# Optimization experiments

Measured on AMD Instinct MI355X. Metric: run time of the kernel, lower is better.

The kernel has to match this reference:

```python
import jax, jax.numpy as jnp
import numpy as np

BETA = 1.0

def setup_inputs() -> dict:
    key = jax.random.key(0)
    k1, k2 = jax.random.split(key)
    z = jax.random.normal(k1, (8, 8192, 64), dtype=jnp.float32)
    # codebook initialized as randn * sc (sc=0.001) in the original module
    codebook = jax.random.normal(k2, (1024, 64), dtype=jnp.float32) * 0.001
    return {"z": z, "codebook": codebook}

def reference(z, codebook):
    # squared euclidean distances: ||z||^2 + ||c||^2 - 2 z.c  -> [B, T, code_num]
    d = (jnp.sum(z ** 2, axis=-1, keepdims=True)
         + jnp.sum(codebook ** 2, axis=1)
         - 2.0 * jnp.einsum('btd,kd->btk', z, codebook))
    min_encoding_indices = jnp.argmin(d, axis=-1)            # [B, T] int
    # one-hot @ codebook is exactly a gather of nearest code vectors
    z_q = codebook[min_encoding_indices]                     # [B, T, D]
    sg = jax.lax.stop_gradient
    loss = jnp.mean((sg(z_q) - z) ** 2) + BETA * jnp.mean((z_q - sg(z)) ** 2)
    # straight-through estimator
    z_q_st = z + sg(z_q - z)
    return (z_q_st, min_encoding_indices, loss)
```

## Files before the change

kernel.cpp:

```cpp
#include <hip/hip_runtime.h>

#define TOKENS 65536
#define DIM 64
#define NCODE 1024
#define MARGIN 1e-5f
#define MARGINS (MARGIN * 2097152.0f)
#define FLAG_CAP 4096
#define TPG 8

#define OUT_IDX_OFF ((size_t)TOKENS * DIM)
#define OUT_LOSS_OFF (OUT_IDX_OFF + TOKENS)

#define WS_LOSS   0
#define WS_FLAGC  8
#define WS_DONEA  12
#define WS_DGRP   16
#define WS_BNORM  2064
#define WS_BNS    6160
#define WS_CHI    10256
#define WS_CLO    141328
#define WS_PACKED 272400
#define WS_FLAGS  337936

typedef __attribute__((ext_vector_type(8))) short short8;
typedef __attribute__((ext_vector_type(8))) _Float16 half8;
typedef __attribute__((ext_vector_type(4))) float f32x4;

static __device__ __forceinline__ half8 as_h8(short8 v) {
    return __builtin_bit_cast(half8, v);
}

__device__ __forceinline__ float np_sumsq64(const float* __restrict__ x) {
#pragma clang fp contract(off)
    float r[8];
#pragma unroll
    for (int j = 0; j < 8; ++j) r[j] = x[j] * x[j];
#pragma unroll
    for (int i = 8; i < 64; i += 8) {
#pragma unroll
        for (int j = 0; j < 8; ++j) {
            float sq = x[i + j] * x[i + j];
            r[j] = r[j] + sq;
        }
    }
    return ((r[0] + r[1]) + (r[2] + r[3])) + ((r[4] + r[5]) + (r[6] + r[7]));
}

__global__ __launch_bounds__(256) void vq_prep(
    const float* __restrict__ cb, unsigned short* __restrict__ chi,
    unsigned short* __restrict__ clo, float* __restrict__ bnorm,
    float* __restrict__ bns,
    unsigned int* __restrict__ ctrl ) {
    int tid = blockIdx.x * 256 + threadIdx.x;
    if (tid < 516) ctrl[tid] = 0u;
    int j = tid & 7;
    int L = (tid >> 3) & 63;
    int cs = tid >> 9;
    int s = cs & 1, c = cs >> 1;
    int code = c * 16 + (L & 15);
    int d = s * 32 + (L >> 4) * 8 + j;
    float v = -8192.0f * cb[(size_t)code * DIM + d];
    _Float16 h = (_Float16)v;
    float hf = (float)h;
    float lo;
    {
#pragma clang fp contract(off)
        lo = v - hf;
    }
    _Float16 l = (_Float16)lo;
    chi[tid] = __builtin_bit_cast(unsigned short, h);
    clo[tid] = __builtin_bit_cast(unsigned short, l);

    if (tid < NCODE) {
        float bn = np_sumsq64(cb + (size_t)tid * DIM);
        bnorm[tid] = bn;
        bns[tid] = bn * 2097152.0f;
    }
}

__device__ __forceinline__ void top2_merge(float& a1, float& a2, int& ai,
                                           float b1, float b2, int bi) {
    float n1 = fminf(a1, b1);
    float n2 = fminf(fmaxf(a1, b1), fminf(a2, b2));
    ai = (b1 < a1) ? bi : ai;
    a1 = n1; a2 = n2;
}

__global__ __launch_bounds__(256, 4) void vq_fast(
    const float* __restrict__ z, const float* __restrict__ cb,
    const unsigned short* __restrict__ cfrag_hi,
    const unsigned short* __restrict__ cfrag_lo,
    const float* __restrict__ bnorm_s, float* __restrict__ out,
    unsigned int* __restrict__ flag_count, int* __restrict__ flag_list,
    unsigned long long* __restrict__ packed_min,
    double* __restrict__ loss_sum, unsigned int flag_cap) {
    __shared__ short8 sh_hi[2][512];
    __shared__ short8 sh_lo[2][512];
    __shared__ float bn_lds[NCODE];
    __shared__ int s_best[64];
    __shared__ int s_flag[64];

    const int tid = threadIdx.x;
    const int lane = tid & 63;
    const int w = tid >> 6;
    const int t0 = blockIdx.x * 64;
    const int tw = t0 + w * 16;
    const int col = lane & 15;
    const int quad = lane >> 4;

    ((float4*)bn_lds)[tid] = ((const float4*)bnorm_s)[tid];

    half8 zhi[2], zlo[2];
#pragma unroll
    for (int s = 0; s < 2; ++s) {
        const float* zp = z + (size_t)(tw + col) * DIM + s * 32 + quad * 8;
        float4 f0 = ((const float4*)zp)[0];
        float4 f1 = ((const float4*)zp)[1];
        float f[8] = {f0.x, f0.y, f0.z, f0.w, f1.x, f1.y, f1.z, f1.w};
        half8 hh8, ll8;
#pragma unroll
        for (int j = 0; j < 8; ++j) {
            float sv = f[j] * 512.0f;
            _Float16 hh = (_Float16)sv;
            float hf = (float)hh;
            float lo;
            {
#pragma clang fp contract(off)
                lo = sv - hf;
            }
            hh8[j] = hh;
            ll8[j] = (_Float16)lo;
        }
        zhi[s] = hh8; zlo[s] = ll8;
    }

    const short8* CH = (const short8*)cfrag_hi;
    const short8* CL = (const short8*)cfrag_lo;

    {
        short8 a0 = CH[tid], a1 = CH[tid + 256];
        short8 b0 = CL[tid], b1 = CL[tid + 256];
        sh_hi[0][tid] = a0; sh_hi[0][tid + 256] = a1;
        sh_lo[0][tid] = b0; sh_lo[0][tid + 256] = b1;
    }
    __syncthreads();

    float m1 = 3.0e38f, m2 = 3.0e38f;
    int bi = 0;
    const int koff = quad * 4;

    for (int g = 0; g < 16; ++g) {
        const int buf = g & 1;
        short8 a0, a1, b0, b1;
        if (g < 15) {
            const int base = (g + 1) * 512 + tid;
            a0 = CH[base]; a1 = CH[base + 256];
            b0 = CL[base]; b1 = CL[base + 256];
        }
#pragma unroll
        for (int cc = 0; cc < 4; ++cc) {
            const int c = g * 4 + cc;
            short8 ch0 = sh_hi[buf][(cc * 2 + 0) * 64 + lane];
            short8 ch1 = sh_hi[buf][(cc * 2 + 1) * 64 + lane];
            short8 cl0 = sh_lo[buf][(cc * 2 + 0) * 64 + lane];
            short8 cl1 = sh_lo[buf][(cc * 2 + 1) * 64 + lane];
            const int cbase = c * 16 + koff;
            const f32x4 bn = *(const f32x4*)&bn_lds[cbase];
            f32x4 acc = bn;
            acc = __builtin_amdgcn_mfma_f32_16x16x32_f16(as_h8(ch0), zhi[0], acc, 0, 0, 0);
            acc = __builtin_amdgcn_mfma_f32_16x16x32_f16(as_h8(cl0), zhi[0], acc, 0, 0, 0);
            acc = __builtin_amdgcn_mfma_f32_16x16x32_f16(as_h8(ch0), zlo[0], acc, 0, 0, 0);
            acc = __builtin_amdgcn_mfma_f32_16x16x32_f16(as_h8(ch1), zhi[1], acc, 0, 0, 0);
            acc = __builtin_amdgcn_mfma_f32_16x16x32_f16(as_h8(cl1), zhi[1], acc, 0, 0, 0);
            acc = __builtin_amdgcn_mfma_f32_16x16x32_f16(as_h8(ch1), zlo[1], acc, 0, 0, 0);
#pragma unroll
            for (int i = 0; i < 4; ++i) {
                float u = acc[i];
                float om1 = m1;
                bool lt = u < om1;
                float fm = fminf(m2, u);
                m2 = lt ? om1 : fm;
                m1 = lt ? u : om1;
                bi = lt ? (cbase + i) : bi;
            }
        }
        if (g < 15) {
            sh_hi[buf ^ 1][tid] = a0; sh_hi[buf ^ 1][tid + 256] = a1;
            sh_lo[buf ^ 1][tid] = b0; sh_lo[buf ^ 1][tid + 256] = b1;
            __syncthreads();
        }
    }

    {
        float a1 = m1, a2 = m2;
        int ai = bi;
        {
            float o1 = __shfl_xor(a1, 16); float o2 = __shfl_xor(a2, 16);
            int oi = __shfl_xor(ai, 16);
            top2_merge(a1, a2, ai, o1, o2, oi);
        }
        {
            float o1 = __shfl_xor(a1, 32); float o2 = __shfl_xor(a2, 32);
            int oi = __shfl_xor(ai, 32);
            top2_merge(a1, a2, ai, o1, o2, oi);
        }
        if (quad == 0) {
            const int slot = w * 16 + col;
            int fl = (a2 - a1) < MARGINS;
            if (fl) {
                unsigned int pos = atomicAdd(flag_count, 1u);
                if (pos >= flag_cap) fl = 0;
                else {
                    flag_list[pos] = t0 + slot;
                    packed_min[pos] = ~0ull;
                }
            }
            s_best[slot] = ai;
            s_flag[slot] = fl;
        }
    }
    __syncthreads();

    const int et = tid >> 1, h = tid & 1;
    float loss_t = 0.0f;
    if (et < 64 && !s_flag[et]) {
        const int B = s_best[et];
        const float4* cq  = (const float4*)(cb + (size_t)B * DIM + h * 32);
        const float4* zq4 = (const float4*)(z + (size_t)(t0 + et) * DIM + h * 32);
        float4* o4 = (float4*)(out + (size_t)(t0 + et) * DIM + h * 32);
#pragma unroll
        for (int jj = 0; jj < 8; ++jj) {
#pragma clang fp contract(off)
            float4 cc = cq[jj];
            float4 zz = zq4[jj];
            float d0 = cc.x - zz.x, d1 = cc.y - zz.y;
            float d2 = cc.z - zz.z, d3 = cc.w - zz.w;
            float4 o;
            o.x = zz.x + d0; o.y = zz.y + d1;
            o.z = zz.z + d2; o.w = zz.w + d3;
            o4[jj] = o;
            loss_t = __fmaf_rn(d0, d0, loss_t);
            loss_t = __fmaf_rn(d1, d1, loss_t);
            loss_t = __fmaf_rn(d2, d2, loss_t);
            loss_t = __fmaf_rn(d3, d3, loss_t);
        }
        if (h == 0) out[OUT_IDX_OFF + t0 + et] = (float)B;
    }
#pragma unroll
    for (int off = 32; off > 0; off >>= 1)
        loss_t += __shfl_down(loss_t, off);
    if (lane == 0 && w < 2) atomicAdd(loss_sum, (double)loss_t);
}

__device__ __forceinline__ unsigned long long shfl_down_u64(unsigned long long v, int off) {
    unsigned int lo = (unsigned int)v, hi = (unsigned int)(v >> 32);
    lo = __shfl_down(lo, off);
    hi = __shfl_down(hi, off);
    return ((unsigned long long)hi << 32) | lo;
}

__global__ __launch_bounds__(256) void vq_exact_min(
    const float* __restrict__ z, const float* __restrict__ cb,
    const float* __restrict__ bnorm,
    const unsigned int* __restrict__ flag_count,
    const int* __restrict__ flag_list,
    unsigned long long* __restrict__ packed_min,
    unsigned int* __restrict__ done_grp, unsigned int* __restrict__ done_all,
    float* __restrict__ out, double* __restrict__ loss_sum,
    unsigned int flag_cap) {
    __shared__ float zsh[TPG * 68];
    __shared__ float szs[TPG];
    __shared__ unsigned int s_old;

    const int tid = threadIdx.x;
    const int w = tid >> 6;
    const int lane = tid & 63;
    unsigned int count = *flag_count;
    if (count > flag_cap) count = flag_cap;
    const unsigned int ngroups = (count + TPG - 1) / TPG;

    if (count == 0) {
        if (blockIdx.x == 0 && tid == 0) {
            double L = atomicAdd(loss_sum, 0.0);
            out[OUT_LOSS_OFF] = (float)(2.0 * L / (double)((size_t)TOKENS * DIM));
        }
        return;
    }

    const int q = blockIdx.x & 3;
    const unsigned int g = blockIdx.x >> 2;
    if (g >= ngroups) return;

    const int k = q * 256 + w * 64 + lane;

    float row[DIM];
    {
        const float4* c4 = (const float4*)(cb + (size_t)k * DIM);
#pragma unroll
        for (int j = 0; j < 16; ++j) {
            float4 v = c4[j];
            row[4 * j + 0] = v.x; row[4 * j + 1] = v.y;
            row[4 * j + 2] = v.z; row[4 * j + 3] = v.w;
        }
    }
    const float bnk = bnorm[k];

    {
        const int i = tid >> 2, part = tid & 3;
        if (i < TPG) {
            const unsigned int li = g * TPG + i;
            if (li < count) {
                const int t = flag_list[li];
                const float4* zp = (const float4*)(z + (size_t)t * DIM + part * 16);
                float4* dst = (float4*)(zsh + i * 68 + part * 16);
#pragma unroll
                for (int e = 0; e < 4; ++e) dst[e] = zp[e];
            }
        }
    }
    __syncthreads();
    if (tid < TPG) szs[tid] = np_sumsq64(zsh + tid * 68);
    __syncthreads();

    for (int tt = 0; tt < TPG; ++tt) {
        const unsigned int li = g * TPG + tt;
        const float* zp = zsh + tt * 68;
        float l16[16];
#pragma unroll
        for (int g2 = 0; g2 < 4; ++g2) {
            float4 v0 = ((const float4*)(zp + 4 * g2))[0];
            float4 v1 = ((const float4*)(zp + 16 + 4 * g2))[0];
            float4 v2 = ((const float4*)(zp + 32 + 4 * g2))[0];
            float4 v3 = ((const float4*)(zp + 48 + 4 * g2))[0];
            float a0[4] = {v0.x, v0.y, v0.z, v0.w};
            float a1[4] = {v1.x, v1.y, v1.z, v1.w};
            float a2[4] = {v2.x, v2.y, v2.z, v2.w};
            float a3[4] = {v3.x, v3.y, v3.z, v3.w};
#pragma unroll
            for (int e = 0; e < 4; ++e) {
#pragma clang fp contract(off)
                int jj = 4 * g2 + e;
                float acc = a3[e] * row[48 + jj];
                acc = __fmaf_rn(a2[e], row[32 + jj], acc);
                acc = __fmaf_rn(a1[e], row[16 + jj], acc);
                acc = __fmaf_rn(a0[e], row[jj],      acc);
                l16[jj] = acc;
            }
        }
        float e_np;
        {
#pragma clang fp contract(off)
#pragma unroll
            for (int jj = 0; jj < 8; ++jj) l16[jj] = l16[jj] + l16[jj + 8];
#pragma unroll
            for (int jj = 0; jj < 4; ++jj) l16[jj] = l16[jj] + l16[jj + 4];
            l16[0] = l16[0] + l16[2];
            l16[1] = l16[1] + l16[3];
            e_np = l16[0] + l16[1];
        }
        float dd;
        {
#pragma clang fp contract(off)
            float t1 = szs[tt] + bnk;
            float mm = 2.0f * e_np;
            dd = t1 - mm;
        }
        unsigned long long pk =
            ((unsigned long long)__float_as_uint(dd) << 10) | (unsigned int)k;
#pragma unroll
        for (int off = 32; off > 0; off >>= 1) {
            unsigned long long o = shfl_down_u64(pk, off);
            pk = (o < pk) ? o : pk;
        }
        if (lane == 0 && li < count)
            atomicMin(&packed_min[li], pk);
    }

    __threadfence();
    __syncthreads();
    if (tid == 0) s_old = atomicAdd(&done_grp[g], 1u);
    __syncthreads();
    if (s_old != 3u) return;
    __threadfence();

    for (int tt = w * (TPG / 4); tt < (w + 1) * (TPG / 4); ++tt) {
        const unsigned int li = g * TPG + tt;
        if (li >= count) break;
        const int t = flag_list[li];
        const unsigned long long pk = atomicAdd(&packed_min[li], 0ull);
        const int best = (int)(pk & 1023ull);
        const float zl = zsh[tt * 68 + lane];
        const float zq = cb[(size_t)best * DIM + lane];
        float d, o;
        {
#pragma clang fp contract(off)
            d = zq - zl;
            o = zl + d;
        }
        out[(size_t)t * DIM + lane] = o;
        float l2 = d * d;
#pragma unroll
        for (int off = 32; off > 0; off >>= 1)
            l2 += __shfl_down(l2, off);
        if (lane == 0) {
            out[OUT_IDX_OFF + t] = (float)best;
            atomicAdd(loss_sum, (double)l2);
        }
    }

    __threadfence();
    __syncthreads();
    if (tid == 0) {
        unsigned int old = atomicAdd(done_all, 1u);
        if (old == ngroups - 1) {
            double L = atomicAdd(loss_sum, 0.0);
            out[OUT_LOSS_OFF] = (float)(2.0 * L / (double)((size_t)TOKENS * DIM));
        }
    }
}

extern "C" void kernel_launch(void* const* d_in, const int* in_sizes, int n_in,
                              void* d_out, int out_size, void* d_ws, size_t ws_size,
                              hipStream_t stream) {
    const float* z  = (const float*)d_in[0];
    const float* cb = (const float*)d_in[1];
    float* out = (float*)d_out;

    char* ws = (char*)d_ws;
    double* loss_sum = (double*)(ws + WS_LOSS);
    unsigned int* flag_count = (unsigned int*)(ws + WS_FLAGC);
    unsigned int* done_all = (unsigned int*)(ws + WS_DONEA);
    unsigned int* done_grp = (unsigned int*)(ws + WS_DGRP);
    float* bnorm = (float*)(ws + WS_BNORM);
    float* bns = (float*)(ws + WS_BNS);
    unsigned short* chi = (unsigned short*)(ws + WS_CHI);
    unsigned short* clo = (unsigned short*)(ws + WS_CLO);
    unsigned long long* packed = (unsigned long long*)(ws + WS_PACKED);
    int* flag_list = (int*)(ws + WS_FLAGS);

    unsigned int cap = 0;
    if (ws_size > WS_FLAGS + 4) {
        size_t c = (ws_size - WS_FLAGS) / 4;
        cap = (c > FLAG_CAP) ? FLAG_CAP : (unsigned int)c;
    }

    vq_prep<<<dim3(256), dim3(256), 0, stream>>>(
        cb, chi, clo, bnorm, bns, (unsigned int*)ws);
    vq_fast<<<dim3(TOKENS / 64), dim3(256), 0, stream>>>(
        z, cb, chi, clo, bns, out, flag_count, flag_list, packed, loss_sum, cap);
    vq_exact_min<<<dim3(2048), dim3(256), 0, stream>>>(
        z, cb, bnorm, flag_count, flag_list, packed, done_grp, done_all,
        out, loss_sum, cap);
}
```

Baseline: 138.4 us.

## Assign one flagged token per block in exact-min fallback kernel

Restructures the exact re-check kernel so each block handles a single flagged token and scans all 1024 codes itself (4 codes per thread), reducing via wave shuffles and shared memory. This drops the cross-block global atomicMin on packed_min and the per-group completion counter. The flag cap doubles and the grid grows to FLAG_CAP blocks. Each block now reloads the full codebook from cache for a single token, so codebook reuse across tokens is lost and the larger grid adds launch cost when few tokens are flagged.

Result: no change. 137.4 us (median of 3 runs) (-0.7%).

```diff
diff --git a/kernel.cpp b/kernel.cpp
--- a/kernel.cpp
+++ b/kernel.cpp
@@ -5,8 +5,7 @@
 #define NCODE 1024
 #define MARGIN 1e-5f
 #define MARGINS (MARGIN * 2097152.0f)
-#define FLAG_CAP 4096
-#define TPG 8
+#define FLAG_CAP 8192
 
 #define OUT_IDX_OFF ((size_t)TOKENS * DIM)
 #define OUT_LOSS_OFF (OUT_IDX_OFF + TOKENS)
@@ -264,20 +263,21 @@
     const float* __restrict__ bnorm,
     const unsigned int* __restrict__ flag_count,
     const int* __restrict__ flag_list,
-    unsigned long long* __restrict__ packed_min,
-    unsigned int* __restrict__ done_grp, unsigned int* __restrict__ done_all,
+    unsigned long long* __restrict__ packed_min ,
+    unsigned int* __restrict__ done_grp ,
+    unsigned int* __restrict__ done_all,
     float* __restrict__ out, double* __restrict__ loss_sum,
     unsigned int flag_cap) {
-    __shared__ float zsh[TPG * 68];
-    __shared__ float szs[TPG];
-    __shared__ unsigned int s_old;
+    __shared__ float zsh[68];
+    __shared__ float s_zs;
+    __shared__ unsigned long long s_pk[4];
+    __shared__ unsigned long long s_min;
 
     const int tid = threadIdx.x;
     const int w = tid >> 6;
     const int lane = tid & 63;
     unsigned int count = *flag_count;
     if (count > flag_cap) count = flag_cap;
-    const unsigned int ngroups = (count + TPG - 1) / TPG;
 
     if (count == 0) {
         if (blockIdx.x == 0 && tid == 0) {
@@ -286,45 +286,38 @@
         }
         return;
     }
-
-    const int q = blockIdx.x & 3;
-    const unsigned int g = blockIdx.x >> 2;
-    if (g >= ngroups) return;
-
-    const int k = q * 256 + w * 64 + lane;
-
-    float row[DIM];
-    {
-        const float4* c4 = (const float4*)(cb + (size_t)k * DIM);
-#pragma unroll
-        for (int j = 0; j < 16; ++j) {
-            float4 v = c4[j];
-            row[4 * j + 0] = v.x; row[4 * j + 1] = v.y;
-            row[4 * j + 2] = v.z; row[4 * j + 3] = v.w;
-        }
-    }
-    const float bnk = bnorm[k];
-
-    {
-        const int i = tid >> 2, part = tid & 3;
-        if (i < TPG) {
-            const unsigned int li = g * TPG + i;
-            if (li < count) {
-                const int t = flag_list[li];
-                const float4* zp = (const float4*)(z + (size_t)t * DIM + part * 16);
-                float4* dst = (float4*)(zsh + i * 68 + part * 16);
-#pragma unroll
-                for (int e = 0; e < 4; ++e) dst[e] = zp[e];
+    if (blockIdx.x >= count) return;
+
+    const int t = flag_list[blockIdx.x];
+
+    if (tid < 4) {
+        const float4* zp = (const float4*)(z + (size_t)t * DIM + tid * 16);
+        float4* dst = (float4*)(zsh + tid * 16);
+#pragma unroll
+        for (int e = 0; e < 4; ++e) dst[e] = zp[e];
+    }
+    __syncthreads();
+    if (tid == 0) s_zs = np_sumsq64(zsh);
+    __syncthreads();
+
+    const float szs = s_zs;
+    const float* zp = zsh;
+    unsigned long long pk = ~0ull;
+
+    for (int e = 0; e < 4; ++e) {
+        const int k = e * 256 + tid;
+        float row[DIM];
+        {
+            const float4* c4 = (const float4*)(cb + (size_t)k * DIM);
+#pragma unroll
+            for (int j = 0; j < 16; ++j) {
+                float4 v = c4[j];
+                row[4 * j + 0] = v.x; row[4 * j + 1] = v.y;
+                row[4 * j + 2] = v.z; row[4 * j + 3] = v.w;
             }
         }
-    }
-    __syncthreads();
-    if (tid < TPG) szs[tid] = np_sumsq64(zsh + tid * 68);
-    __syncthreads();
-
-    for (int tt = 0; tt < TPG; ++tt) {
-        const unsigned int li = g * TPG + tt;
-        const float* zp = zsh + tt * 68;
+        const float bnk = bnorm[k];
+
         float l16[16];
 #pragma unroll
         for (int g2 = 0; g2 < 4; ++g2) {
@@ -337,13 +330,13 @@
             float a2[4] = {v2.x, v2.y, v2.z, v2.w};
             float a3[4] = {v3.x, v3.y, v3.z, v3.w};
 #pragma unroll
-            for (int e = 0; e < 4; ++e) {
-#pragma clang fp contract(off)
-                int jj = 4 * g2 + e;
-                float acc = a3[e] * row[48 + jj];
-                acc = __fmaf_rn(a2[e], row[32 + jj], acc);
-                acc = __fmaf_rn(a1[e], row[16 + jj], acc);
-                acc = __fmaf_rn(a0[e], row[jj],      acc);
+            for (int ee = 0; ee < 4; ++ee) {
+#pragma clang fp contract(off)
+                int jj = 4 * g2 + ee;
+                float acc = a3[ee] * row[48 + jj];
+                acc = __fmaf_rn(a2[ee], row[32 + jj], acc);
+                acc = __fmaf_rn(a1[ee], row[16 + jj], acc);
+                acc = __fmaf_rn(a0[ee], row[jj],      acc);
                 l16[jj] = acc;
             }
         }
@@ -361,35 +354,34 @@
         float dd;
         {
 #pragma clang fp contract(off)
-            float t1 = szs[tt] + bnk;
+            float t1 = szs + bnk;
             float mm = 2.0f * e_np;
             dd = t1 - mm;
         }
-        unsigned long long pk =
+        unsigned long long p =
             ((unsigned long long)__float_as_uint(dd) << 10) | (unsigned int)k;
-#pragma unroll
-        for (int off = 32; off > 0; off >>= 1) {
-            unsigned long long o = shfl_down_u64(pk, off);
-            pk = (o < pk) ? o : pk;
-        }
-        if (lane == 0 && li < count)
-            atomicMin(&packed_min[li], pk);
-    }
-
-    __threadfence();
-    __syncthreads();
-    if (tid == 0) s_old = atomicAdd(&done_grp[g], 1u);
-    __syncthreads();
-    if (s_old != 3u) return;
-    __threadfence();
-
-    for (int tt = w * (TPG / 4); tt < (w + 1) * (TPG / 4); ++tt) {
-        const unsigned int li = g * TPG + tt;
-        if (li >= count) break;
-        const int t = flag_list[li];
-        const unsigned long long pk = atomicAdd(&packed_min[li], 0ull);
-        const int best = (int)(pk & 1023ull);
-        const float zl = zsh[tt * 68 + lane];
+        pk = (p < pk) ? p : pk;
+    }
+
+#pragma unroll
+    for (int off = 32; off > 0; off >>= 1) {
+        unsigned long long o = shfl_down_u64(pk, off);
+        pk = (o < pk) ? o : pk;
+    }
+    if (lane == 0) s_pk[w] = pk;
+    __syncthreads();
+    if (tid == 0) {
+        unsigned long long m = s_pk[0];
+        m = (s_pk[1] < m) ? s_pk[1] : m;
+        m = (s_pk[2] < m) ? s_pk[2] : m;
+        m = (s_pk[3] < m) ? s_pk[3] : m;
+        s_min = m;
+    }
+    __syncthreads();
+
+    if (w == 0) {
+        const int best = (int)(s_min & 1023ull);
+        const float zl = zsh[lane];
         const float zq = cb[(size_t)best * DIM + lane];
         float d, o;
         {
@@ -412,7 +404,7 @@
     __syncthreads();
     if (tid == 0) {
         unsigned int old = atomicAdd(done_all, 1u);
-        if (old == ngroups - 1) {
+        if (old == count - 1) {
             double L = atomicAdd(loss_sum, 0.0);
             out[OUT_LOSS_OFF] = (float)(2.0 * L / (double)((size_t)TOKENS * DIM));
         }
@@ -448,7 +440,7 @@
         cb, chi, clo, bnorm, bns, (unsigned int*)ws);
     vq_fast<<<dim3(TOKENS / 64), dim3(256), 0, stream>>>(
         z, cb, chi, clo, bns, out, flag_count, flag_list, packed, loss_sum, cap);
-    vq_exact_min<<<dim3(2048), dim3(256), 0, stream>>>(
+    vq_exact_min<<<dim3(FLAG_CAP), dim3(256), 0, stream>>>(
         z, cb, bnorm, flag_count, flag_list, packed, done_grp, done_all,
         out, loss_sum, cap);
 }
```
